# Performance work log

Measured on AMD Instinct MI355X. Metric: run time of the kernel, lower is better.

## Reference

```python
import jax, jax.numpy as jnp
import numpy as np

TEMPERATURE = 0.5


def setup_inputs() -> dict:
    key = jax.random.key(0)
    k1, k2 = jax.random.split(key)
    B, D = 4096, 256
    return {
        "features": jax.random.normal(k1, (B, D), dtype=jnp.float32),
        "transformed_features": jax.random.normal(k2, (B, D), dtype=jnp.float32),
    }


def reference(features, transformed_features):
    B = features.shape[0]
    N = 2 * B
    all_features = jnp.concatenate([features, transformed_features], axis=0)  # [2B, D]
    # F.normalize(dim=-1): L2 normalize with eps clamp of 1e-12 on the norm
    norm = jnp.maximum(jnp.linalg.norm(all_features, axis=-1, keepdims=True), 1e-12)
    all_features = all_features / norm
    sim = jnp.matmul(all_features, all_features.T)  # [2B, 2B]
    # positive pairs: diag at offsets +B and -B
    pos = jnp.concatenate([jnp.diagonal(sim, offset=B), jnp.diagonal(sim, offset=-B)], axis=0)  # [2B]
    numerator = jnp.exp(pos / TEMPERATURE)
    # torch code multiplies sim by (1 - eye) BEFORE exp, so diagonal contributes exp(0)=1 to the sum
    sim_no_diag = sim * (1.0 - jnp.eye(N, dtype=sim.dtype))
    denominator = jnp.exp(sim_no_diag / TEMPERATURE).sum(axis=1)  # [2B]
    losses = -jnp.log(numerator / denominator)
    return jnp.sum(losses) / N
```

## Files before the change

kernel.cpp:

```cpp
#include <hip/hip_runtime.h>

#define B_ROWS 4096
#define N_ROWS 8192
#define DDIM   256
#define IT2    2.885390081777927f

#define BM 128
#define BK 64
#define NTILE 64
#define NBLK  2080
#define NPARTS 128

typedef unsigned short ushort_t;
typedef __bf16 bf16x8 __attribute__((ext_vector_type(8)));
typedef float  f32x4  __attribute__((ext_vector_type(4)));

__device__ __forceinline__ ushort_t f2bf(float x) {
    union { float f; unsigned u; } a; a.f = x;
    unsigned r = a.u + 0x7fffu + ((a.u >> 16) & 1u);
    return (ushort_t)(r >> 16);
}

__device__ __forceinline__ void gload_lds16(const void* g, void* l) {
    __builtin_amdgcn_global_load_lds(
        (const __attribute__((address_space(1))) unsigned int*)g,
        (__attribute__((address_space(3))) unsigned int*)l,
        16, 0, 0);
}

__global__ __launch_bounds__(256) void k_norm_pos(
        const float* __restrict__ feats, const float* __restrict__ tfeats,
        ushort_t* __restrict__ Xb, float* __restrict__ posv) {
    __shared__ float fbuf[2][DDIM];
    __shared__ float nsh[4];
    int w = threadIdx.x >> 6, l = threadIdx.x & 63;
    int i0 = blockIdx.x * 2;
    int pair = (w < 2) ? w : (w - 2);
    int row  = (w < 2) ? (i0 + pair) : (i0 + pair + B_ROWS);
    const float* src = (w < 2) ? feats + (size_t)(i0 + pair) * DDIM
                               : tfeats + (size_t)(i0 + pair) * DDIM;
    float4 v = ((const float4*)src)[l];
    float ss = v.x*v.x + v.y*v.y + v.z*v.z + v.w*v.w;
    #pragma unroll
    for (int m = 1; m < 64; m <<= 1) ss += __shfl_xor(ss, m);
    float nrm = fmaxf(sqrtf(ss), 1e-12f);
    float inv = 1.0f / nrm;
    ushort4 o;
    o.x = f2bf(v.x * inv); o.y = f2bf(v.y * inv);
    o.z = f2bf(v.z * inv); o.w = f2bf(v.w * inv);
    ((ushort4*)(Xb + (size_t)row * DDIM))[l] = o;
    if (w < 2) ((float4*)fbuf[pair])[l] = v;
    if (l == 0) nsh[w] = nrm;
    __syncthreads();
    if (w >= 2) {
        float4 a = ((const float4*)fbuf[pair])[l];
        float d = a.x*v.x + a.y*v.y + a.z*v.z + a.w*v.w;
        #pragma unroll
        for (int m = 1; m < 64; m <<= 1) d += __shfl_xor(d, m);
        if (l == 0) posv[i0 + pair] = d / (nsh[pair] * nsh[w]);
    }
}

__global__ __launch_bounds__(256) void k_gemm(
        const ushort_t* __restrict__ Xb, float* __restrict__ parts) {
    __shared__ ushort_t ldsA[BM * BK];
    __shared__ ushort_t ldsB[BM * BK];

    int idx = blockIdx.x;
    int rt = 0;
    while (idx >= (NTILE - rt)) { idx -= (NTILE - rt); rt++; }
    int ct = rt + idx;
    bool isdiag = (rt == ct);

    int rowbase = rt * BM;
    int colbase = ct * BM;
    int t = threadIdx.x;
    int l = t & 63;
    int w = t >> 6;
    int wm = w >> 1, wn = w & 1;

    f32x4 acc[4][4];
    #pragma unroll
    for (int m = 0; m < 4; m++)
        #pragma unroll
        for (int n = 0; n < 4; n++) acc[m][n] = (f32x4){0.f, 0.f, 0.f, 0.f};

    for (int kb = 0; kb < DDIM; kb += BK) {
        #pragma unroll
        for (int i = 0; i < 4; i++) {
            int o   = (i * 256 + t) * 16;
            int row = o >> 7;
            int cb  = o & 127;
            int scb = cb ^ ((row & 7) << 4);
            const char* ga = (const char*)Xb +
                ((size_t)(rowbase + row) * DDIM + kb) * 2 + scb;
            gload_lds16(ga, (char*)ldsA + o);
            const char* gb = (const char*)Xb +
                ((size_t)(colbase + row) * DDIM + kb) * 2 + scb;
            gload_lds16(gb, (char*)ldsB + o);
        }
        __syncthreads();

        #pragma unroll
        for (int ks = 0; ks < 2; ks++) {
            bf16x8 af[4], bfr[4];
            int cbw = ((l >> 4) * 16) + ks * 64;
            #pragma unroll
            for (int m = 0; m < 4; m++) {
                int row  = wm * 64 + m * 16 + (l & 15);
                int addr = row * 128 + (cbw ^ ((row & 7) << 4));
                af[m] = *(const bf16x8*)((const char*)ldsA + addr);
            }
            #pragma unroll
            for (int n = 0; n < 4; n++) {
                int row  = wn * 64 + n * 16 + (l & 15);
                int addr = row * 128 + (cbw ^ ((row & 7) << 4));
                bfr[n] = *(const bf16x8*)((const char*)ldsB + addr);
            }
            #pragma unroll
            for (int m = 0; m < 4; m++)
                #pragma unroll
                for (int n = 0; n < 4; n++)
                    acc[m][n] = __builtin_amdgcn_mfma_f32_16x16x32_bf16(
                        af[m], bfr[n], acc[m][n], 0, 0, 0);
        }
        __syncthreads();
    }

    float rs[4][4];
    float cs[4];
    #pragma unroll
    for (int m = 0; m < 4; m++)
        #pragma unroll
        for (int j = 0; j < 4; j++) rs[m][j] = 0.0f;
    #pragma unroll
    for (int n = 0; n < 4; n++) cs[n] = 0.0f;

    #pragma unroll
    for (int m = 0; m < 4; m++) {
        #pragma unroll
        for (int j = 0; j < 4; j++) {
            int grow = rowbase + wm * 64 + m * 16 + (l >> 4) * 4 + j;
            #pragma unroll
            for (int n = 0; n < 4; n++) {
                int gcol = colbase + wn * 64 + n * 16 + (l & 15);
                float e = exp2f(acc[m][n][j] * IT2);
                if (isdiag && grow == gcol) e = 1.0f;
                rs[m][j] += e;
                cs[n]    += e;
            }
        }
    }

    #pragma unroll
    for (int m = 0; m < 4; m++)
        #pragma unroll
        for (int j = 0; j < 4; j++) {
            float v = rs[m][j];
            v += __shfl_xor(v, 1);
            v += __shfl_xor(v, 2);
            v += __shfl_xor(v, 4);
            v += __shfl_xor(v, 8);
            if ((l & 15) == 0) {
                int grow = rowbase + wm * 64 + m * 16 + (l >> 4) * 4 + j;
                parts[(size_t)(ct * 2 + wn) * N_ROWS + grow] = v;
            }
        }

    if (!isdiag) {
        #pragma unroll
        for (int n = 0; n < 4; n++) {
            float v = cs[n];
            v += __shfl_xor(v, 16);
            v += __shfl_xor(v, 32);
            if (l < 16) {
                int gcol = colbase + wn * 64 + n * 16 + l;
                parts[(size_t)(rt * 2 + wm) * N_ROWS + gcol] = v;
            }
        }
    }
}

__global__ __launch_bounds__(256) void k_rowreduce(
        const float* __restrict__ parts, float* __restrict__ bsums) {
    int row = blockIdx.x * 256 + threadIdx.x;
    float den = 0.0f;
    #pragma unroll 8
    for (int p = 0; p < NPARTS; p++) den += parts[(size_t)p * N_ROWS + row];
    float v = logf(den);
    #pragma unroll
    for (int m = 1; m < 64; m <<= 1) v += __shfl_xor(v, m);
    __shared__ float red[4];
    if ((threadIdx.x & 63) == 0) red[threadIdx.x >> 6] = v;
    __syncthreads();
    if (threadIdx.x == 0)
        bsums[blockIdx.x] = red[0] + red[1] + red[2] + red[3];
}

__global__ __launch_bounds__(256) void k_final(
        const float* __restrict__ bsums, const float* __restrict__ posv,
        float* __restrict__ out) {
    int t = threadIdx.x;
    float ps = 0.0f;
    for (int i = t; i < B_ROWS; i += 256) ps += posv[i];
    float lg = (t < 32) ? bsums[t] : 0.0f;
    float comb = lg - 4.0f * ps;
    #pragma unroll
    for (int m = 1; m < 64; m <<= 1) comb += __shfl_xor(comb, m);
    __shared__ float red[4];
    if ((t & 63) == 0) red[t >> 6] = comb;
    __syncthreads();
    if (t == 0) out[0] = (red[0] + red[1] + red[2] + red[3]) / (float)N_ROWS;
}

extern "C" void kernel_launch(void* const* d_in, const int* in_sizes, int n_in,
                              void* d_out, int out_size, void* d_ws, size_t ws_size,
                              hipStream_t stream) {
    const float* feats  = (const float*)d_in[0];
    const float* tfeats = (const float*)d_in[1];
    float* out = (float*)d_out;
    char* ws = (char*)d_ws;

    ushort_t* Xb    = (ushort_t*)ws;
    float*    posv  = (float*)(ws + 4194304);
    float*    parts = (float*)(ws + 4210688);
    float*    bsums = (float*)(ws + 8404992);

    k_norm_pos <<<B_ROWS / 2, 256, 0, stream>>>(feats, tfeats, Xb, posv);
    k_gemm     <<<NBLK, 256, 0, stream>>>(Xb, parts);
    k_rowreduce<<<N_ROWS / 256, 256, 0, stream>>>(parts, bsums);
    k_final    <<<1, 256, 0, stream>>>(bsums, posv, out);
}
```

Before: 115.9 us.

## Fuse row reduction and final loss into GEMM via atomics and last-block ticket

Replaces the per-tile partial-sum buffer and the two follow-up reduction kernels with atomicAdd accumulation into four per-row denominator slices. The last GEMM block to finish, detected with a ticket counter, computes the log-sum and the final loss. The GEMM K-loop also gains double-buffered LDS staging so global-to-LDS loads overlap MFMA compute. In exchange it adds atomic contention, a fence, a serial tail in one block, and twice the LDS per block, which may lower occupancy.

```diff
diff --git a/kernel.cpp b/kernel.cpp
--- a/kernel.cpp
+++ b/kernel.cpp
@@ -5,11 +5,8 @@
 #define DDIM   256
 #define IT2    2.885390081777927f
 
-#define BM 128
-#define BK 64
-#define NTILE 64
-#define NBLK  2080
-#define NPARTS 128
+#define NTILE   64
+#define NBLKTRI 2080
 
 typedef unsigned short ushort_t;
 typedef __bf16 bf16x8 __attribute__((ext_vector_type(8)));
@@ -28,13 +25,20 @@
         16, 0, 0);
 }
 
-__global__ __launch_bounds__(256) void k_norm_pos(
+__global__ __launch_bounds__(256) void k_prep(
         const float* __restrict__ feats, const float* __restrict__ tfeats,
-        ushort_t* __restrict__ Xb, float* __restrict__ posv) {
+        ushort_t* __restrict__ Xb, float* __restrict__ posv,
+        float* __restrict__ den4, int* __restrict__ ticket) {
     __shared__ float fbuf[2][DDIM];
     __shared__ float nsh[4];
     int w = threadIdx.x >> 6, l = threadIdx.x & 63;
-    int i0 = blockIdx.x * 2;
+    int bid = blockIdx.x;
+    int i0 = bid * 2;
+
+    int z = bid * 256 + threadIdx.x;
+    if (z < 4 * N_ROWS) den4[z] = 0.0f;
+    if (z == 4 * N_ROWS) *ticket = 0;
+
     int pair = (w < 2) ? w : (w - 2);
     int row  = (w < 2) ? (i0 + pair) : (i0 + pair + B_ROWS);
     const float* src = (w < 2) ? feats + (size_t)(i0 + pair) * DDIM
@@ -61,23 +65,40 @@
     }
 }
 
-__global__ __launch_bounds__(256) void k_gemm(
-        const ushort_t* __restrict__ Xb, float* __restrict__ parts) {
-    __shared__ ushort_t ldsA[BM * BK];
-    __shared__ ushort_t ldsB[BM * BK];
-
-    int idx = blockIdx.x;
-    int rt = 0;
+__global__ __launch_bounds__(256) void k_main(
+        const ushort_t* __restrict__ Xb, const float* __restrict__ posv,
+        float* __restrict__ den4, int* __restrict__ ticket,
+        float* __restrict__ out) {
+    __shared__ ushort_t lds[2][2][128 * 64];
+    __shared__ float red[4];
+    __shared__ int islast;
+
+    const int t = threadIdx.x, l = t & 63, w = t >> 6;
+    const int wm = w >> 1, wn = w & 1;
+
+    int idx = blockIdx.x, rt = 0;
     while (idx >= (NTILE - rt)) { idx -= (NTILE - rt); rt++; }
-    int ct = rt + idx;
-    bool isdiag = (rt == ct);
-
-    int rowbase = rt * BM;
-    int colbase = ct * BM;
-    int t = threadIdx.x;
-    int l = t & 63;
-    int w = t >> 6;
-    int wm = w >> 1, wn = w & 1;
+    const int ct = rt + idx;
+    const bool isdiag = (rt == ct);
+    const int rowbase = rt * 128;
+    const int colbase = ct * 128;
+
+    #define STAGE(buf, kb)                                                   \
+        do {                                                                 \
+            _Pragma("unroll")                                                \
+            for (int i = 0; i < 4; i++) {                                    \
+                int o   = (i * 256 + t) * 16;                                \
+                int row = o >> 7;                                            \
+                int cb  = o & 127;                                           \
+                int scb = cb ^ ((row & 7) << 4);                             \
+                gload_lds16((const char*)Xb +                                \
+                    ((size_t)(rowbase + row) * DDIM + (kb) * 64) * 2 + scb,  \
+                    (char*)lds[buf][0] + o);                                 \
+                gload_lds16((const char*)Xb +                                \
+                    ((size_t)(colbase + row) * DDIM + (kb) * 64) * 2 + scb,  \
+                    (char*)lds[buf][1] + o);                                 \
+            }                                                                \
+        } while (0)
 
     f32x4 acc[4][4];
     #pragma unroll
@@ -85,21 +106,13 @@
         #pragma unroll
         for (int n = 0; n < 4; n++) acc[m][n] = (f32x4){0.f, 0.f, 0.f, 0.f};
 
-    for (int kb = 0; kb < DDIM; kb += BK) {
-        #pragma unroll
-        for (int i = 0; i < 4; i++) {
-            int o   = (i * 256 + t) * 16;
-            int row = o >> 7;
-            int cb  = o & 127;
-            int scb = cb ^ ((row & 7) << 4);
-            const char* ga = (const char*)Xb +
-                ((size_t)(rowbase + row) * DDIM + kb) * 2 + scb;
-            gload_lds16(ga, (char*)ldsA + o);
-            const char* gb = (const char*)Xb +
-                ((size_t)(colbase + row) * DDIM + kb) * 2 + scb;
-            gload_lds16(gb, (char*)ldsB + o);
-        }
-        __syncthreads();
+    STAGE(0, 0);
+    __syncthreads();
+
+    #pragma unroll
+    for (int kb = 0; kb < 4; kb++) {
+        const int buf = kb & 1;
+        if (kb < 3) STAGE(buf ^ 1, kb + 1);
 
         #pragma unroll
         for (int ks = 0; ks < 2; ks++) {
@@ -109,13 +122,13 @@
             for (int m = 0; m < 4; m++) {
                 int row  = wm * 64 + m * 16 + (l & 15);
                 int addr = row * 128 + (cbw ^ ((row & 7) << 4));
-                af[m] = *(const bf16x8*)((const char*)ldsA + addr);
+                af[m] = *(const bf16x8*)((const char*)lds[buf][0] + addr);
             }
             #pragma unroll
             for (int n = 0; n < 4; n++) {
                 int row  = wn * 64 + n * 16 + (l & 15);
                 int addr = row * 128 + (cbw ^ ((row & 7) << 4));
-                bfr[n] = *(const bf16x8*)((const char*)ldsB + addr);
+                bfr[n] = *(const bf16x8*)((const char*)lds[buf][1] + addr);
             }
             #pragma unroll
             for (int m = 0; m < 4; m++)
@@ -128,13 +141,11 @@
     }
 
     float rs[4][4];
-    float cs[4];
+    float cs[4] = {0.f, 0.f, 0.f, 0.f};
     #pragma unroll
     for (int m = 0; m < 4; m++)
         #pragma unroll
         for (int j = 0; j < 4; j++) rs[m][j] = 0.0f;
-    #pragma unroll
-    for (int n = 0; n < 4; n++) cs[n] = 0.0f;
 
     #pragma unroll
     for (int m = 0; m < 4; m++) {
@@ -157,16 +168,13 @@
         #pragma unroll
         for (int j = 0; j < 4; j++) {
             float v = rs[m][j];
-            v += __shfl_xor(v, 1);
-            v += __shfl_xor(v, 2);
-            v += __shfl_xor(v, 4);
-            v += __shfl_xor(v, 8);
+            v += __shfl_xor(v, 1); v += __shfl_xor(v, 2);
+            v += __shfl_xor(v, 4); v += __shfl_xor(v, 8);
             if ((l & 15) == 0) {
                 int grow = rowbase + wm * 64 + m * 16 + (l >> 4) * 4 + j;
-                parts[(size_t)(ct * 2 + wn) * N_ROWS + grow] = v;
-            }
-        }
-
+                atomicAdd(&den4[(size_t)wn * N_ROWS + grow], v);
+            }
+        }
     if (!isdiag) {
         #pragma unroll
         for (int n = 0; n < 4; n++) {
@@ -175,40 +183,31 @@
             v += __shfl_xor(v, 32);
             if (l < 16) {
                 int gcol = colbase + wn * 64 + n * 16 + l;
-                parts[(size_t)(rt * 2 + wm) * N_ROWS + gcol] = v;
-            }
-        }
-    }
-}
-
-__global__ __launch_bounds__(256) void k_rowreduce(
-        const float* __restrict__ parts, float* __restrict__ bsums) {
-    int row = blockIdx.x * 256 + threadIdx.x;
-    float den = 0.0f;
-    #pragma unroll 8
-    for (int p = 0; p < NPARTS; p++) den += parts[(size_t)p * N_ROWS + row];
-    float v = logf(den);
-    #pragma unroll
-    for (int m = 1; m < 64; m <<= 1) v += __shfl_xor(v, m);
-    __shared__ float red[4];
-    if ((threadIdx.x & 63) == 0) red[threadIdx.x >> 6] = v;
-    __syncthreads();
-    if (threadIdx.x == 0)
-        bsums[blockIdx.x] = red[0] + red[1] + red[2] + red[3];
-}
-
-__global__ __launch_bounds__(256) void k_final(
-        const float* __restrict__ bsums, const float* __restrict__ posv,
-        float* __restrict__ out) {
-    int t = threadIdx.x;
-    float ps = 0.0f;
-    for (int i = t; i < B_ROWS; i += 256) ps += posv[i];
-    float lg = (t < 32) ? bsums[t] : 0.0f;
-    float comb = lg - 4.0f * ps;
+                atomicAdd(&den4[(size_t)(2 + wm) * N_ROWS + gcol], v);
+            }
+        }
+    }
+
+    __threadfence();
+    if (t == 0) islast = (atomicAdd(ticket, 1) == NBLKTRI - 1);
+    __syncthreads();
+    if (!islast) return;
+
+    float lsum = 0.0f;
+    for (int r = t; r < N_ROWS; r += 256) {
+        float d = 0.0f;
+        #pragma unroll
+        for (int s = 0; s < 4; s++)
+            d += __hip_atomic_load(&den4[(size_t)s * N_ROWS + r],
+                                   __ATOMIC_RELAXED, __HIP_MEMORY_SCOPE_AGENT);
+        lsum += logf(d);
+    }
+    float psum = 0.0f;
+    for (int i = t; i < B_ROWS; i += 256) psum += posv[i];
+    float comb = lsum - 4.0f * psum;
     #pragma unroll
     for (int m = 1; m < 64; m <<= 1) comb += __shfl_xor(comb, m);
-    __shared__ float red[4];
-    if ((t & 63) == 0) red[t >> 6] = comb;
+    if (l == 0) red[w] = comb;
     __syncthreads();
     if (t == 0) out[0] = (red[0] + red[1] + red[2] + red[3]) / (float)N_ROWS;
 }
@@ -221,13 +220,11 @@
     float* out = (float*)d_out;
     char* ws = (char*)d_ws;
 
-    ushort_t* Xb    = (ushort_t*)ws;
-    float*    posv  = (float*)(ws + 4194304);
-    float*    parts = (float*)(ws + 4210688);
-    float*    bsums = (float*)(ws + 8404992);
-
-    k_norm_pos <<<B_ROWS / 2, 256, 0, stream>>>(feats, tfeats, Xb, posv);
-    k_gemm     <<<NBLK, 256, 0, stream>>>(Xb, parts);
-    k_rowreduce<<<N_ROWS / 256, 256, 0, stream>>>(parts, bsums);
-    k_final    <<<1, 256, 0, stream>>>(bsums, posv, out);
-}
+    ushort_t* Xb     = (ushort_t*)ws;
+    float*    posv   = (float*)(ws + 4194304);
+    float*    den4   = (float*)(ws + 4210688);
+    int*      ticket = (int*)(ws + 4341760);
+
+    k_prep<<<B_ROWS / 2, 256, 0, stream>>>(feats, tfeats, Xb, posv, den4, ticket);
+    k_main<<<NBLKTRI, 256, 0, stream>>>(Xb, posv, den4, ticket, out);
+}
```

Measured after the change: 235.9 us. 104% more time.
